# Kernel optimization log

Measured on AMD Instinct MI355X. Metric: run time of the kernel, lower is better.

The kernel has to match this reference:

```python
import jax, jax.numpy as jnp
import numpy as np

N_NODES = 50000
N_EDGES = 600000
D = 128
NUM_LAYERS = 2
ALPHA = 0.5
EPS = 1e-12  # torch F.normalize eps


def setup_inputs() -> dict:
    key = jax.random.key(0)
    k1, k2, k3, k4, k5 = jax.random.split(key, 5)
    x = jax.random.normal(k1, (N_NODES, D), dtype=jnp.float32)
    edge_attr = jax.random.normal(k2, (N_EDGES, D), dtype=jnp.float32)
    question_emb = jax.random.normal(k3, (D,), dtype=jnp.float32)
    src = jax.random.randint(k4, (N_EDGES,), 0, N_NODES)
    dst = jax.random.randint(k5, (N_EDGES,), 0, N_NODES)
    edge_index = jnp.stack([src, dst], axis=0).astype(jnp.int64)
    return {"x": x, "edge_attr": edge_attr, "question_emb": question_emb, "edge_index": edge_index}


def reference(x, edge_attr, question_emb, edge_index):
    num_nodes = x.shape[0]
    # edge similarity: cosine of edge_attr rows vs question vector
    ea = edge_attr / jnp.maximum(jnp.linalg.norm(edge_attr, axis=1, keepdims=True), EPS)
    q = question_emb / jnp.maximum(jnp.linalg.norm(question_emb), EPS)
    edge_sim = ea @ q  # [E]
    src, dst = edge_index[0], edge_index[1]
    # degree of destination nodes (constant across layers)
    deg = jax.ops.segment_sum(jnp.ones_like(edge_sim), dst, num_segments=num_nodes)
    deg = jnp.clip(deg, 1.0)[:, None]  # [N,1]
    for _ in range(NUM_LAYERS):
        msgs = x[src] * edge_sim[:, None]                              # [E,D] gather + scale
        x_new = jax.ops.segment_sum(msgs, dst, num_segments=num_nodes)  # [N,D] scatter-add
        x_new = x_new / deg                                             # mean aggregation
        x = ALPHA * x + (1.0 - ALPHA) * x_new                           # residual blend
    return x
```

## Files before the change

### kernel.cpp

```cpp
#include <hip/hip_runtime.h>
#include <math.h>

#define N_NODES 50000
#define N_EDGES 600000
#define D 128
#define EPS 1e-12f

#define SCAN_B 256
#define N_SCAN_BLOCKS ((N_NODES + SCAN_B - 1) / SCAN_B)

__global__ void qnorm_kernel(const float* __restrict__ q, float* __restrict__ qn) {
    __shared__ float red[2];
    int t = threadIdx.x;
    float v = q[t];
    float ss = v * v;
    #pragma unroll
    for (int off = 32; off > 0; off >>= 1) ss += __shfl_down(ss, off);
    if ((t & 63) == 0) red[t >> 6] = ss;
    __syncthreads();
    float inv = 1.0f / fmaxf(sqrtf(red[0] + red[1]), EPS);
    qn[t] = v * inv;
}

__global__ void edge_sim_kernel(const float* __restrict__ ea,
                                const float* __restrict__ qn,
                                const int* __restrict__ dst,
                                float* __restrict__ sim,
                                int* __restrict__ cnt) {
    int gid  = blockIdx.x * blockDim.x + threadIdx.x;
    int wave = gid >> 6;
    if (wave >= N_EDGES / 2) return;
    int lane = threadIdx.x & 63;
    int half = lane >> 5;
    int l32  = lane & 31;
    int e    = 2 * wave + half;

    float4 v = ((const float4*)(ea + (size_t)e * D))[l32];
    float4 q = ((const float4*)qn)[l32];
    float dot = v.x * q.x + v.y * q.y + v.z * q.z + v.w * q.w;
    float ss  = v.x * v.x + v.y * v.y + v.z * v.z + v.w * v.w;
    #pragma unroll
    for (int off = 16; off > 0; off >>= 1) {
        dot += __shfl_xor(dot, off);
        ss  += __shfl_xor(ss, off);
    }
    if (l32 == 0) {
        sim[e] = dot / fmaxf(sqrtf(ss), EPS);
        atomicAdd(&cnt[dst[e]], 1);
    }
}

__global__ void block_sum_kernel(const int* __restrict__ cnt, int* __restrict__ bsum) {
    __shared__ int s[SCAN_B];
    int t = threadIdx.x;
    int i = blockIdx.x * SCAN_B + t;
    s[t] = (i < N_NODES) ? cnt[i] : 0;
    __syncthreads();
    for (int off = SCAN_B / 2; off > 0; off >>= 1) {
        if (t < off) s[t] += s[t + off];
        __syncthreads();
    }
    if (t == 0) bsum[blockIdx.x] = s[0];
}

__global__ void scan_bsums_kernel(int* __restrict__ bsum) {
    __shared__ int s[SCAN_B];
    int t = threadIdx.x;
    int v = (t < N_SCAN_BLOCKS) ? bsum[t] : 0;
    s[t] = v;
    __syncthreads();
    for (int off = 1; off < SCAN_B; off <<= 1) {
        int a = (t >= off) ? s[t - off] : 0;
        __syncthreads();
        s[t] += a;
        __syncthreads();
    }
    if (t < N_SCAN_BLOCKS) bsum[t] = s[t] - v;
}

__global__ void scan_final_kernel(const int* __restrict__ cnt,
                                  const int* __restrict__ bsum,
                                  int* __restrict__ row_ptr,
                                  int* __restrict__ cursor,
                                  float* __restrict__ deg_inv) {
    __shared__ int s[SCAN_B];
    int t = threadIdx.x;
    int i = blockIdx.x * SCAN_B + t;
    int v = (i < N_NODES) ? cnt[i] : 0;
    s[t] = v;
    __syncthreads();
    for (int off = 1; off < SCAN_B; off <<= 1) {
        int a = (t >= off) ? s[t - off] : 0;
        __syncthreads();
        s[t] += a;
        __syncthreads();
    }
    if (i < N_NODES) {
        int rp = s[t] - v + bsum[blockIdx.x];
        row_ptr[i] = rp;
        cursor[i]  = rp;
        deg_inv[i] = 1.0f / fmaxf((float)v, 1.0f);
    }
    if (i == N_NODES - 1) row_ptr[N_NODES] = N_EDGES;
}

__global__ void fill_kernel(const int* __restrict__ src, const int* __restrict__ dst,
                            const float* __restrict__ sim,
                            int* __restrict__ cursor,
                            int* __restrict__ csr_src, float* __restrict__ csr_sim) {
    int e = blockIdx.x * blockDim.x + threadIdx.x;
    if (e >= N_EDGES) return;
    int d = dst[e];
    int idx = atomicAdd(&cursor[d], 1);
    csr_src[idx] = src[e];
    csr_sim[idx] = sim[e];
}

__global__ void agg_kernel(const float* __restrict__ xin,
                           const int* __restrict__ row_ptr,
                           const int* __restrict__ csr_src,
                           const float* __restrict__ csr_sim,
                           const float* __restrict__ deg_inv,
                           float* __restrict__ xout) {
    int gid  = blockIdx.x * blockDim.x + threadIdx.x;
    int node = gid >> 6;
    if (node >= N_NODES) return;
    int lane = threadIdx.x & 63;
    int half = lane >> 5;
    int l32  = lane & 31;

    int beg = row_ptr[node];
    int end = row_ptr[node + 1];
    int n   = end - beg;

    int   sl = 0; float wl = 0.0f;
    if (lane < n) { sl = csr_src[beg + lane]; wl = csr_sim[beg + lane]; }

    float4 acc = make_float4(0.0f, 0.0f, 0.0f, 0.0f);
    int nn = (n < 64) ? n : 64;
    #pragma unroll 2
    for (int j = half; j < nn; j += 2) {
        int   s = __shfl(sl, j);
        float w = __shfl(wl, j);
        float4 v = ((const float4*)(xin + (size_t)s * D))[l32];
        acc.x += v.x * w; acc.y += v.y * w; acc.z += v.z * w; acc.w += v.w * w;
    }
    for (int j = 64 + half; j < n; j += 2) {
        int   s = csr_src[beg + j];
        float w = csr_sim[beg + j];
        float4 v = ((const float4*)(xin + (size_t)s * D))[l32];
        acc.x += v.x * w; acc.y += v.y * w; acc.z += v.z * w; acc.w += v.w * w;
    }
    acc.x += __shfl_xor(acc.x, 32);
    acc.y += __shfl_xor(acc.y, 32);
    acc.z += __shfl_xor(acc.z, 32);
    acc.w += __shfl_xor(acc.w, 32);

    if (half == 0) {
        float di = deg_inv[node];
        float4 a = ((const float4*)(xin + (size_t)node * D))[l32];
        float4 o;
        o.x = 0.5f * a.x + 0.5f * acc.x * di;
        o.y = 0.5f * a.y + 0.5f * acc.y * di;
        o.z = 0.5f * a.z + 0.5f * acc.z * di;
        o.w = 0.5f * a.w + 0.5f * acc.w * di;
        ((float4*)(xout + (size_t)node * D))[l32] = o;
    }
}

extern "C" void kernel_launch(void* const* d_in, const int* in_sizes, int n_in,
                              void* d_out, int out_size, void* d_ws, size_t ws_size,
                              hipStream_t stream) {
    const float* x  = (const float*)d_in[0];
    const float* ea = (const float*)d_in[1];
    const float* q  = (const float*)d_in[2];
    const int*   ei = (const int*)d_in[3];
    const int* src = ei;
    const int* dst = ei + N_EDGES;
    float* out = (float*)d_out;

    float* x1       = (float*)d_ws;
    float* sim      = x1 + (size_t)N_NODES * D;
    float* csr_sim  = sim + N_EDGES;
    float* deg_inv  = csr_sim + N_EDGES;
    float* qn       = deg_inv + N_NODES;
    int*   cnt      = (int*)(qn + 128);
    int*   row_ptr  = cnt + N_NODES;
    int*   cursor   = row_ptr + N_NODES + 1;
    int*   bsum     = cursor + N_NODES;
    int*   csr_src  = bsum + 256;

    hipMemsetAsync(cnt, 0, (size_t)N_NODES * sizeof(int), stream);

    qnorm_kernel<<<1, 128, 0, stream>>>(q, qn);

    {
        long long threads = (long long)(N_EDGES / 2) * 64;
        int blocks = (int)((threads + 255) / 256);
        edge_sim_kernel<<<blocks, 256, 0, stream>>>(ea, qn, dst, sim, cnt);
    }

    block_sum_kernel<<<N_SCAN_BLOCKS, SCAN_B, 0, stream>>>(cnt, bsum);
    scan_bsums_kernel<<<1, SCAN_B, 0, stream>>>(bsum);
    scan_final_kernel<<<N_SCAN_BLOCKS, SCAN_B, 0, stream>>>(cnt, bsum, row_ptr, cursor, deg_inv);

    fill_kernel<<<(N_EDGES + 255) / 256, 256, 0, stream>>>(src, dst, sim, cursor, csr_src, csr_sim);

    const int agg_blocks = (int)(((long long)N_NODES * 64 + 255) / 256);
    agg_kernel<<<agg_blocks, 256, 0, stream>>>(x,  row_ptr, csr_src, csr_sim, deg_inv, x1);
    agg_kernel<<<agg_blocks, 256, 0, stream>>>(x1, row_ptr, csr_src, csr_sim, deg_inv, out);
}
```

Baseline: 557.4 us.

## Split feature dimension into 16-column chunks across blocks in aggregation

Restructures the aggregation kernel so each block handles one 16-float column chunk of four nodes, with eight chunk-blocks per node group. Inside a wave, four groups of 16 lanes each process a different edge and read scalar floats. The partial sums are combined with two shuffles, and the output uses nontemporal stores. The aim is to raise parallelism and improve L2 locality per column slice, at the cost of reading the CSR row eight times and issuing narrower 64-byte gathers instead of float4 loads.

```diff
diff --git a/kernel.cpp b/kernel.cpp
--- a/kernel.cpp
+++ b/kernel.cpp
@@ -122,49 +122,46 @@
                            const float* __restrict__ csr_sim,
                            const float* __restrict__ deg_inv,
                            float* __restrict__ xout) {
-    int gid  = blockIdx.x * blockDim.x + threadIdx.x;
-    int node = gid >> 6;
+    int bid   = blockIdx.x;
+    int chunk = bid & 7;
+    int group = bid >> 3;
+    int wid   = threadIdx.x >> 6;
+    int node  = group * 4 + wid;
     if (node >= N_NODES) return;
     int lane = threadIdx.x & 63;
-    int half = lane >> 5;
-    int l32  = lane & 31;
+    int g    = lane >> 4;
+    int l16  = lane & 15;
 
     int beg = row_ptr[node];
-    int end = row_ptr[node + 1];
-    int n   = end - beg;
-
-    int   sl = 0; float wl = 0.0f;
-    if (lane < n) { sl = csr_src[beg + lane]; wl = csr_sim[beg + lane]; }
-
-    float4 acc = make_float4(0.0f, 0.0f, 0.0f, 0.0f);
-    int nn = (n < 64) ? n : 64;
+    int n   = row_ptr[node + 1] - beg;
+
+    int   sl = node; float wl = 0.0f;
+    int nc = (n < 64) ? n : 64;
+    if (lane < nc) { sl = csr_src[beg + lane]; wl = csr_sim[beg + lane]; }
+
+    const float* xc = xin + (size_t)chunk * 16 + l16;
+    float acc = 0.0f;
+    int nn4 = (nc + 3) & ~3;
     #pragma unroll 2
-    for (int j = half; j < nn; j += 2) {
-        int   s = __shfl(sl, j);
-        float w = __shfl(wl, j);
-        float4 v = ((const float4*)(xin + (size_t)s * D))[l32];
-        acc.x += v.x * w; acc.y += v.y * w; acc.z += v.z * w; acc.w += v.w * w;
-    }
-    for (int j = 64 + half; j < n; j += 2) {
-        int   s = csr_src[beg + j];
-        float w = csr_sim[beg + j];
-        float4 v = ((const float4*)(xin + (size_t)s * D))[l32];
-        acc.x += v.x * w; acc.y += v.y * w; acc.z += v.z * w; acc.w += v.w * w;
-    }
-    acc.x += __shfl_xor(acc.x, 32);
-    acc.y += __shfl_xor(acc.y, 32);
-    acc.z += __shfl_xor(acc.z, 32);
-    acc.w += __shfl_xor(acc.w, 32);
-
-    if (half == 0) {
-        float di = deg_inv[node];
-        float4 a = ((const float4*)(xin + (size_t)node * D))[l32];
-        float4 o;
-        o.x = 0.5f * a.x + 0.5f * acc.x * di;
-        o.y = 0.5f * a.y + 0.5f * acc.y * di;
-        o.z = 0.5f * a.z + 0.5f * acc.z * di;
-        o.w = 0.5f * a.w + 0.5f * acc.w * di;
-        ((float4*)(xout + (size_t)node * D))[l32] = o;
+    for (int j = 0; j < nn4; j += 4) {
+        int   s = __shfl(sl, j + g);
+        float w = __shfl(wl, j + g);
+        acc += xc[(size_t)s * D] * w;
+    }
+    for (int j = 64; j < n; j += 4) {
+        int jj = j + g;
+        int   s = (jj < n) ? csr_src[beg + jj] : node;
+        float w = (jj < n) ? csr_sim[beg + jj] : 0.0f;
+        acc += xc[(size_t)s * D] * w;
+    }
+    acc += __shfl_xor(acc, 16);
+    acc += __shfl_xor(acc, 32);
+
+    if (lane < 16) {
+        size_t o = (size_t)node * D + chunk * 16 + lane;
+        float a  = xin[o];
+        float r  = 0.5f * a + 0.5f * acc * deg_inv[node];
+        __builtin_nontemporal_store(r, &xout[o]);
     }
 }
 
@@ -206,7 +203,7 @@
 
     fill_kernel<<<(N_EDGES + 255) / 256, 256, 0, stream>>>(src, dst, sim, cursor, csr_src, csr_sim);
 
-    const int agg_blocks = (int)(((long long)N_NODES * 64 + 255) / 256);
+    const int agg_blocks = (N_NODES / 4) * 8;
     agg_kernel<<<agg_blocks, 256, 0, stream>>>(x,  row_ptr, csr_src, csr_sim, deg_inv, x1);
     agg_kernel<<<agg_blocks, 256, 0, stream>>>(x1, row_ptr, csr_src, csr_sim, deg_inv, out);
 }
```

New measurement: 756.2 us. 1.36x slower.

## Replace CSR build with fixed-capacity per-node buckets and overflow list

Applied to the files above, without the earlier changes.

Removes the scan kernels and the separate fill pass by appending each edge's (src, sim) pair directly into a fixed 64-slot bucket per destination node inside the edge-similarity kernel. Edges beyond the capacity go to an overflow list that a single-block kernel applies after each aggregation layer. The query norm is now recomputed per wave inside the edge kernel, so the separate qnorm launch is gone. This cuts kernel launches and passes over the edges, at the cost of a large sparse bucket array that the aggregation reads with strided access.

```diff
diff --git a/kernel.cpp b/kernel.cpp
--- a/kernel.cpp
+++ b/kernel.cpp
@@ -5,28 +5,16 @@
 #define N_EDGES 600000
 #define D 128
 #define EPS 1e-12f
+#define CAP 64
 
-#define SCAN_B 256
-#define N_SCAN_BLOCKS ((N_NODES + SCAN_B - 1) / SCAN_B)
-
-__global__ void qnorm_kernel(const float* __restrict__ q, float* __restrict__ qn) {
-    __shared__ float red[2];
-    int t = threadIdx.x;
-    float v = q[t];
-    float ss = v * v;
-    #pragma unroll
-    for (int off = 32; off > 0; off >>= 1) ss += __shfl_down(ss, off);
-    if ((t & 63) == 0) red[t >> 6] = ss;
-    __syncthreads();
-    float inv = 1.0f / fmaxf(sqrtf(red[0] + red[1]), EPS);
-    qn[t] = v * inv;
-}
-
-__global__ void edge_sim_kernel(const float* __restrict__ ea,
-                                const float* __restrict__ qn,
-                                const int* __restrict__ dst,
-                                float* __restrict__ sim,
-                                int* __restrict__ cnt) {
+__global__ void edge_fill_kernel(const float* __restrict__ ea,
+                                 const float* __restrict__ q,
+                                 const int* __restrict__ src,
+                                 const int* __restrict__ dst,
+                                 int* __restrict__ cnt,
+                                 int2* __restrict__ bucket,
+                                 int* __restrict__ ovf_cnt,
+                                 int4* __restrict__ ovf) {
     int gid  = blockIdx.x * blockDim.x + threadIdx.x;
     int wave = gid >> 6;
     if (wave >= N_EDGES / 2) return;
@@ -35,92 +23,33 @@
     int l32  = lane & 31;
     int e    = 2 * wave + half;
 
-    float4 v = ((const float4*)(ea + (size_t)e * D))[l32];
-    float4 q = ((const float4*)qn)[l32];
-    float dot = v.x * q.x + v.y * q.y + v.z * q.z + v.w * q.w;
+    float4 v  = ((const float4*)(ea + (size_t)e * D))[l32];
+    float4 qv = ((const float4*)q)[l32];
+    float dot = v.x * qv.x + v.y * qv.y + v.z * qv.z + v.w * qv.w;
     float ss  = v.x * v.x + v.y * v.y + v.z * v.z + v.w * v.w;
+    float qs  = qv.x * qv.x + qv.y * qv.y + qv.z * qv.z + qv.w * qv.w;
     #pragma unroll
     for (int off = 16; off > 0; off >>= 1) {
         dot += __shfl_xor(dot, off);
         ss  += __shfl_xor(ss, off);
+        qs  += __shfl_xor(qs, off);
     }
     if (l32 == 0) {
-        sim[e] = dot / fmaxf(sqrtf(ss), EPS);
-        atomicAdd(&cnt[dst[e]], 1);
+        float sim = dot / (fmaxf(sqrtf(ss), EPS) * fmaxf(sqrtf(qs), EPS));
+        int d    = dst[e];
+        int slot = atomicAdd(&cnt[d], 1);
+        if (slot < CAP) {
+            bucket[(size_t)d * CAP + slot] = make_int2(src[e], __float_as_int(sim));
+        } else {
+            int oi = atomicAdd(ovf_cnt, 1);
+            ovf[oi] = make_int4(d, src[e], __float_as_int(sim), 0);
+        }
     }
 }
 
-__global__ void block_sum_kernel(const int* __restrict__ cnt, int* __restrict__ bsum) {
-    __shared__ int s[SCAN_B];
-    int t = threadIdx.x;
-    int i = blockIdx.x * SCAN_B + t;
-    s[t] = (i < N_NODES) ? cnt[i] : 0;
-    __syncthreads();
-    for (int off = SCAN_B / 2; off > 0; off >>= 1) {
-        if (t < off) s[t] += s[t + off];
-        __syncthreads();
-    }
-    if (t == 0) bsum[blockIdx.x] = s[0];
-}
-
-__global__ void scan_bsums_kernel(int* __restrict__ bsum) {
-    __shared__ int s[SCAN_B];
-    int t = threadIdx.x;
-    int v = (t < N_SCAN_BLOCKS) ? bsum[t] : 0;
-    s[t] = v;
-    __syncthreads();
-    for (int off = 1; off < SCAN_B; off <<= 1) {
-        int a = (t >= off) ? s[t - off] : 0;
-        __syncthreads();
-        s[t] += a;
-        __syncthreads();
-    }
-    if (t < N_SCAN_BLOCKS) bsum[t] = s[t] - v;
-}
-
-__global__ void scan_final_kernel(const int* __restrict__ cnt,
-                                  const int* __restrict__ bsum,
-                                  int* __restrict__ row_ptr,
-                                  int* __restrict__ cursor,
-                                  float* __restrict__ deg_inv) {
-    __shared__ int s[SCAN_B];
-    int t = threadIdx.x;
-    int i = blockIdx.x * SCAN_B + t;
-    int v = (i < N_NODES) ? cnt[i] : 0;
-    s[t] = v;
-    __syncthreads();
-    for (int off = 1; off < SCAN_B; off <<= 1) {
-        int a = (t >= off) ? s[t - off] : 0;
-        __syncthreads();
-        s[t] += a;
-        __syncthreads();
-    }
-    if (i < N_NODES) {
-        int rp = s[t] - v + bsum[blockIdx.x];
-        row_ptr[i] = rp;
-        cursor[i]  = rp;
-        deg_inv[i] = 1.0f / fmaxf((float)v, 1.0f);
-    }
-    if (i == N_NODES - 1) row_ptr[N_NODES] = N_EDGES;
-}
-
-__global__ void fill_kernel(const int* __restrict__ src, const int* __restrict__ dst,
-                            const float* __restrict__ sim,
-                            int* __restrict__ cursor,
-                            int* __restrict__ csr_src, float* __restrict__ csr_sim) {
-    int e = blockIdx.x * blockDim.x + threadIdx.x;
-    if (e >= N_EDGES) return;
-    int d = dst[e];
-    int idx = atomicAdd(&cursor[d], 1);
-    csr_src[idx] = src[e];
-    csr_sim[idx] = sim[e];
-}
-
 __global__ void agg_kernel(const float* __restrict__ xin,
-                           const int* __restrict__ row_ptr,
-                           const int* __restrict__ csr_src,
-                           const float* __restrict__ csr_sim,
-                           const float* __restrict__ deg_inv,
+                           const int* __restrict__ cnt,
+                           const int2* __restrict__ bucket,
                            float* __restrict__ xout) {
     int gid  = blockIdx.x * blockDim.x + threadIdx.x;
     int node = gid >> 6;
@@ -129,25 +58,20 @@
     int half = lane >> 5;
     int l32  = lane & 31;
 
-    int beg = row_ptr[node];
-    int end = row_ptr[node + 1];
-    int n   = end - beg;
+    int n  = cnt[node];
+    int nb = (n < CAP) ? n : CAP;
 
-    int   sl = 0; float wl = 0.0f;
-    if (lane < n) { sl = csr_src[beg + lane]; wl = csr_sim[beg + lane]; }
+    int sl = 0; float wl = 0.0f;
+    if (lane < nb) {
+        int2 p = bucket[(size_t)node * CAP + lane];
+        sl = p.x; wl = __int_as_float(p.y);
+    }
 
     float4 acc = make_float4(0.0f, 0.0f, 0.0f, 0.0f);
-    int nn = (n < 64) ? n : 64;
     #pragma unroll 2
-    for (int j = half; j < nn; j += 2) {
+    for (int j = half; j < nb; j += 2) {
         int   s = __shfl(sl, j);
         float w = __shfl(wl, j);
-        float4 v = ((const float4*)(xin + (size_t)s * D))[l32];
-        acc.x += v.x * w; acc.y += v.y * w; acc.z += v.z * w; acc.w += v.w * w;
-    }
-    for (int j = 64 + half; j < n; j += 2) {
-        int   s = csr_src[beg + j];
-        float w = csr_sim[beg + j];
         float4 v = ((const float4*)(xin + (size_t)s * D))[l32];
         acc.x += v.x * w; acc.y += v.y * w; acc.z += v.z * w; acc.w += v.w * w;
     }
@@ -157,7 +81,7 @@
     acc.w += __shfl_xor(acc.w, 32);
 
     if (half == 0) {
-        float di = deg_inv[node];
+        float di = 1.0f / fmaxf((float)n, 1.0f);
         float4 a = ((const float4*)(xin + (size_t)node * D))[l32];
         float4 o;
         o.x = 0.5f * a.x + 0.5f * acc.x * di;
@@ -165,6 +89,22 @@
         o.z = 0.5f * a.z + 0.5f * acc.z * di;
         o.w = 0.5f * a.w + 0.5f * acc.w * di;
         ((float4*)(xout + (size_t)node * D))[l32] = o;
+    }
+}
+
+__global__ void ovf_fix_kernel(const float* __restrict__ xin,
+                               const int* __restrict__ cnt,
+                               const int* __restrict__ ovf_cnt,
+                               const int4* __restrict__ ovf,
+                               float* __restrict__ xout) {
+    int t = threadIdx.x;
+    int m = *ovf_cnt;
+    for (int i = 0; i < m; ++i) {
+        int4 p = ovf[i];
+        int d = p.x, s = p.y;
+        float w  = __int_as_float(p.z);
+        float di = 1.0f / fmaxf((float)cnt[d], 1.0f);
+        xout[(size_t)d * D + t] += 0.5f * w * di * xin[(size_t)s * D + t];
     }
 }
 
@@ -179,34 +119,24 @@
     const int* dst = ei + N_EDGES;
     float* out = (float*)d_out;
 
-    float* x1       = (float*)d_ws;
-    float* sim      = x1 + (size_t)N_NODES * D;
-    float* csr_sim  = sim + N_EDGES;
-    float* deg_inv  = csr_sim + N_EDGES;
-    float* qn       = deg_inv + N_NODES;
-    int*   cnt      = (int*)(qn + 128);
-    int*   row_ptr  = cnt + N_NODES;
-    int*   cursor   = row_ptr + N_NODES + 1;
-    int*   bsum     = cursor + N_NODES;
-    int*   csr_src  = bsum + 256;
+    float* x1      = (float*)d_ws;
+    int2*  bucket  = (int2*)(x1 + (size_t)N_NODES * D);
+    int*   cnt     = (int*)(bucket + (size_t)N_NODES * CAP);
+    int*   ovf_cnt = cnt + N_NODES;
+    int4*  ovf     = (int4*)(cnt + N_NODES + 4);
 
-    hipMemsetAsync(cnt, 0, (size_t)N_NODES * sizeof(int), stream);
-
-    qnorm_kernel<<<1, 128, 0, stream>>>(q, qn);
+    hipMemsetAsync(cnt, 0, (size_t)(N_NODES + 4) * sizeof(int), stream);
 
     {
         long long threads = (long long)(N_EDGES / 2) * 64;
         int blocks = (int)((threads + 255) / 256);
-        edge_sim_kernel<<<blocks, 256, 0, stream>>>(ea, qn, dst, sim, cnt);
+        edge_fill_kernel<<<blocks, 256, 0, stream>>>(ea, q, src, dst,
+                                                     cnt, bucket, ovf_cnt, ovf);
     }
 
-    block_sum_kernel<<<N_SCAN_BLOCKS, SCAN_B, 0, stream>>>(cnt, bsum);
-    scan_bsums_kernel<<<1, SCAN_B, 0, stream>>>(bsum);
-    scan_final_kernel<<<N_SCAN_BLOCKS, SCAN_B, 0, stream>>>(cnt, bsum, row_ptr, cursor, deg_inv);
-
-    fill_kernel<<<(N_EDGES + 255) / 256, 256, 0, stream>>>(src, dst, sim, cursor, csr_src, csr_sim);
-
     const int agg_blocks = (int)(((long long)N_NODES * 64 + 255) / 256);
-    agg_kernel<<<agg_blocks, 256, 0, stream>>>(x,  row_ptr, csr_src, csr_sim, deg_inv, x1);
-    agg_kernel<<<agg_blocks, 256, 0, stream>>>(x1, row_ptr, csr_src, csr_sim, deg_inv, out);
+    agg_kernel<<<agg_blocks, 256, 0, stream>>>(x,  cnt, bucket, x1);
+    ovf_fix_kernel<<<1, 128, 0, stream>>>(x,  cnt, ovf_cnt, ovf, x1);
+    agg_kernel<<<agg_blocks, 256, 0, stream>>>(x1, cnt, bucket, out);
+    ovf_fix_kernel<<<1, 128, 0, stream>>>(x1, cnt, ovf_cnt, ovf, out);
 }
```

New measurement: 541.5 us. -2.9%, faster.
